# Kernel optimization log

Measured on AMD Instinct MI355X. Metric: run time of the kernel, lower is better.

## Reference

```python
import jax, jax.numpy as jnp
import numpy as np

# dims
A, T, K, H, NH, F, L = 64, 50, 6, 128, 8, 60, 512
M = A * T * K          # 19200 mode nodes (layout: agent, time, mode)
AT = A * T             # 3200 agent-timestep nodes
NL = 10                # GA layers: t2m,l2m,m2m_h,m2m_a,m2m_s,t2n,l2n,n2n_h,n2n_a,n2n_s
FF = 4 * H
E = 150000


def _ln(x, g, b):
    mu = x.mean(-1, keepdims=True)
    var = jnp.mean((x - mu) ** 2, axis=-1, keepdims=True)
    return (x - mu) * jax.lax.rsqrt(var + 1e-5) * g + b


def _mlp(x, W1, b1, W2, b2):
    return jax.nn.relu(x @ W1 + b1) @ W2 + b2


def _edge_emb(attr, i, eW1, eb1, eW2, eb2):
    # pad raw edge features to width 5 so all embed MLPs share a stacked param layout
    x = jnp.pad(attr, ((0, 0), (0, 5 - attr.shape[-1])))
    return jax.nn.relu(x @ eW1[i] + eb1[i]) @ eW2[i] + eb2[i]


def _segment_softmax(scores, dst, n):
    smax = jax.ops.segment_max(scores, dst, num_segments=n)
    smax = jnp.where(jnp.isfinite(smax), smax, 0.0)
    ex = jnp.exp(scores - smax[dst])
    den = jax.ops.segment_sum(ex, dst, num_segments=n)
    return ex / (den[dst] + 1e-9)


def _graph_attention(i, x_src, x_dst, ei, edge_emb, p):
    (Wq, Wk, Wv, Wo, Wke, Wve, g1, b1, g2, b2, fW1, fb1, fW2, fb2) = p
    src, dst = ei[0], ei[1]
    dh = H // NH
    n_dst = x_dst.shape[0]
    xd = _ln(x_dst, g1[i], b1[i])
    xs = _ln(x_src, g1[i], b1[i])
    q = (xd @ Wq[i]).reshape(n_dst, NH, dh)
    k = (xs @ Wk[i])[src]            # gather per-edge keys  [E,H]
    v = (xs @ Wv[i])[src]
    if edge_emb is not None:
        k = k + edge_emb @ Wke[i]
        v = v + edge_emb @ Wve[i]
    k = k.reshape(-1, NH, dh)
    v = v.reshape(-1, NH, dh)
    scores = jnp.sum(q[dst] * k, axis=-1) / np.sqrt(dh)   # [E,NH]
    attn = _segment_softmax(scores, dst, n_dst)
    agg = jax.ops.segment_sum(attn[..., None] * v, dst, num_segments=n_dst)
    x = x_dst + agg.reshape(n_dst, H) @ Wo[i]
    h = _ln(x, g2[i], b2[i])
    return x + _mlp(h, fW1[i], fb1[i], fW2[i], fb2[i])


def _forward(a_input, l_embs, mode_tokens,
             emb_W1, emb_b1, emb_W2, emb_b2,
             ga_Wq, ga_Wk, ga_Wv, ga_Wo, ga_Wke, ga_Wve,
             ga_g1, ga_b1, ga_g2, ga_b2, ga_fW1, ga_fb1, ga_fW2, ga_fb2,
             tp_W1, tp_b1, tp_W2, tp_b2,
             pa_W1, pa_b1, pa_W2, pa_b2,
             tr_W1, tr_b1, tr_W2, tr_b2,
             t2m_attr, l2m_attr, m2m_h_attr, m2m_a_attr,
             t2m_ei, l2m_ei, m2m_h_ei, m2m_a_ei, m2m_s_ei):
    ga = (ga_Wq, ga_Wk, ga_Wv, ga_Wo, ga_Wke, ga_Wve,
          ga_g1, ga_b1, ga_g2, ga_b2, ga_fW1, ga_fb1, ga_fW2, ga_fb2)
    # agent embedding: TwoLayerMLP on [vel_len, vel_theta, length, width, type]
    a_embs = (jax.nn.relu(a_input @ emb_W1[0] + emb_b1[0]) @ emb_W2[0] + emb_b2[0]).reshape(AT, H)
    # mode tokens broadcast over (agent, time)
    m = jnp.broadcast_to(mode_tokens, (A, T, K, H)).reshape(M, H)
    # edge-attr embeddings (gather-compute pattern)
    t2m_e = _edge_emb(t2m_attr, 1, emb_W1, emb_b1, emb_W2, emb_b2)
    l2m_e = _edge_emb(l2m_attr, 2, emb_W1, emb_b1, emb_W2, emb_b2)
    m2m_h_e = _edge_emb(m2m_h_attr, 3, emb_W1, emb_b1, emb_W2, emb_b2)
    m2m_a_e = _edge_emb(m2m_a_attr, 4, emb_W1, emb_b1, emb_W2, emb_b2)
    # proposal stage
    m = _graph_attention(0, a_embs, m, t2m_ei, t2m_e, ga)
    m = _graph_attention(1, l_embs, m, l2m_ei, l2m_e, ga)
    m = _graph_attention(2, m, m, m2m_h_ei, m2m_h_e, ga)
    m = _graph_attention(3, m, m, m2m_a_ei, m2m_a_e, ga)
    m = _graph_attention(4, m, m, m2m_s_ei, None, ga)
    m_last = m.reshape(A, T, K, H)[:, -1]                 # [A,K,H]
    proposal = _mlp(m_last, tp_W1, tp_b1, tp_W2, tp_b2)   # [A,K,2F]
    anchor = _mlp(proposal, pa_W1, pa_b1, pa_W2, pa_b2)   # [A,K,H]
    # refinement stage on anchor-conditioned mode nodes
    n = (m.reshape(A, T, K, H) + anchor[:, None]).reshape(M, H)
    n = _graph_attention(5, a_embs, n, t2m_ei, t2m_e, ga)
    n = _graph_attention(6, l_embs, n, l2m_ei, l2m_e, ga)
    n = _graph_attention(7, n, n, m2m_h_ei, m2m_h_e, ga)
    n = _graph_attention(8, n, n, m2m_a_ei, m2m_a_e, ga)
    n = _graph_attention(9, n, n, m2m_s_ei, None, ga)
    n_last = n.reshape(A, T, K, H)[:, -1]
    refine = proposal + _mlp(n_last, tr_W1, tr_b1, tr_W2, tr_b2)
    return jnp.stack([proposal, refine])                  # [2,A,K,2F]


def setup_inputs() -> dict:
    key = jax.random.key(0)
    ks = list(jax.random.split(key, 64))
    it = iter(ks)
    nx = lambda: next(it)
    p = lambda *s: 0.02 * jax.random.normal(nx(), s, dtype=jnp.float32)
    inp = {}
    inp['a_input'] = jax.random.normal(nx(), (A, T, 5), dtype=jnp.float32)
    inp['l_embs'] = jax.random.normal(nx(), (L, H), dtype=jnp.float32)
    inp['mode_tokens'] = p(K, H)
    # stacked edge/feature embed MLPs: 0:a,1:t2m,2:l2m,3:m2m_h,4:m2m_a
    inp['emb_W1'] = p(5, 5, H); inp['emb_b1'] = jnp.zeros((5, H), jnp.float32)
    inp['emb_W2'] = p(5, H, H); inp['emb_b2'] = jnp.zeros((5, H), jnp.float32)
    # stacked GraphAttention params
    for nm in ['ga_Wq', 'ga_Wk', 'ga_Wv', 'ga_Wo', 'ga_Wke', 'ga_Wve']:
        inp[nm] = p(NL, H, H)
    inp['ga_g1'] = jnp.ones((NL, H), jnp.float32); inp['ga_b1'] = jnp.zeros((NL, H), jnp.float32)
    inp['ga_g2'] = jnp.ones((NL, H), jnp.float32); inp['ga_b2'] = jnp.zeros((NL, H), jnp.float32)
    inp['ga_fW1'] = p(NL, H, FF); inp['ga_fb1'] = jnp.zeros((NL, FF), jnp.float32)
    inp['ga_fW2'] = p(NL, FF, H); inp['ga_fb2'] = jnp.zeros((NL, H), jnp.float32)
    # heads
    inp['tp_W1'] = p(H, H); inp['tp_b1'] = jnp.zeros((H,), jnp.float32)
    inp['tp_W2'] = p(H, 2 * F); inp['tp_b2'] = jnp.zeros((2 * F,), jnp.float32)
    inp['pa_W1'] = p(2 * F, H); inp['pa_b1'] = jnp.zeros((H,), jnp.float32)
    inp['pa_W2'] = p(H, H); inp['pa_b2'] = jnp.zeros((H,), jnp.float32)
    inp['tr_W1'] = p(H, H); inp['tr_b1'] = jnp.zeros((H,), jnp.float32)
    inp['tr_W2'] = p(H, 2 * F); inp['tr_b2'] = jnp.zeros((2 * F,), jnp.float32)
    # raw edge features
    inp['t2m_attr'] = jax.random.normal(nx(), (E, 4), dtype=jnp.float32)
    inp['l2m_attr'] = jax.random.normal(nx(), (E, 3), dtype=jnp.float32)
    inp['m2m_h_attr'] = jax.random.normal(nx(), (E, 4), dtype=jnp.float32)
    inp['m2m_a_attr'] = jax.random.normal(nx(), (E, 3), dtype=jnp.float32)
    # edge indices (src row range differs per graph)
    ri = lambda hi: jax.random.randint(nx(), (E,), 0, hi, dtype=jnp.int32)
    inp['t2m_ei'] = jnp.stack([ri(AT), ri(M)])
    inp['l2m_ei'] = jnp.stack([ri(L), ri(M)])
    inp['m2m_h_ei'] = jnp.stack([ri(M), ri(M)])
    inp['m2m_a_ei'] = jnp.stack([ri(M), ri(M)])
    inp['m2m_s_ei'] = jnp.stack([ri(M), ri(M)])
    return inp


def reference(a_input, l_embs, mode_tokens,
              emb_W1, emb_b1, emb_W2, emb_b2,
              ga_Wq, ga_Wk, ga_Wv, ga_Wo, ga_Wke, ga_Wve,
              ga_g1, ga_b1, ga_g2, ga_b2, ga_fW1, ga_fb1, ga_fW2, ga_fb2,
              tp_W1, tp_b1, tp_W2, tp_b2,
              pa_W1, pa_b1, pa_W2, pa_b2,
              tr_W1, tr_b1, tr_W2, tr_b2,
              t2m_attr, l2m_attr, m2m_h_attr, m2m_a_attr,
              t2m_ei, l2m_ei, m2m_h_ei, m2m_a_ei, m2m_s_ei):
    return _forward(a_input, l_embs, mode_tokens,
                    emb_W1, emb_b1, emb_W2, emb_b2,
                    ga_Wq, ga_Wk, ga_Wv, ga_Wo, ga_Wke, ga_Wve,
                    ga_g1, ga_b1, ga_g2, ga_b2, ga_fW1, ga_fb1, ga_fW2, ga_fb2,
                    tp_W1, tp_b1, tp_W2, tp_b2,
                    pa_W1, pa_b1, pa_W2, pa_b2,
                    tr_W1, tr_b1, tr_W2, tr_b2,
                    t2m_attr, l2m_attr, m2m_h_attr, m2m_a_attr,
                    t2m_ei, l2m_ei, m2m_h_ei, m2m_a_ei, m2m_s_ei)
```

## Files before the change

kernel.cpp:

```cpp
#include <hip/hip_runtime.h>
#include <hip/hip_bf16.h>
#include <math.h>

#define DEV __device__ __forceinline__

typedef __attribute__((ext_vector_type(4))) float floatx4;
typedef __attribute__((ext_vector_type(8))) __bf16 bf16x8;

static constexpr int A_ = 64, T_ = 50, K_ = 6, H_ = 128, NH_ = 8, F_ = 60, L_ = 512;
static constexpr int M_  = A_ * T_ * K_;
static constexpr int AT_ = A_ * T_;
static constexpr int FF_ = 4 * H_;
static constexpr int NL_ = 10;
static constexpr int P2F = 2 * F_;
static constexpr int AK_ = A_ * K_;
static constexpr size_t WLAY = 196608;

DEV ushort f2bh(float f) {
    unsigned u = __float_as_uint(f);
    unsigned r = u + 0x7FFFu + ((u >> 16) & 1u);
    return (ushort)(r >> 16);
}
DEV float bh2f(ushort h) { return __uint_as_float(((unsigned)h) << 16); }

__global__ __launch_bounds__(256) void ln_kernel(const float* __restrict__ x,
                                                 const float* __restrict__ g,
                                                 const float* __restrict__ b,
                                                 float* __restrict__ y, int n) {
    int row = blockIdx.x * 4 + (threadIdx.x >> 6);
    int lane = threadIdx.x & 63;
    if (row >= n) return;
    const float* xr = x + (size_t)row * H_;
    float v0 = xr[lane], v1 = xr[lane + 64];
    float s = v0 + v1;
    for (int m = 32; m >= 1; m >>= 1) s += __shfl_xor(s, m, 64);
    float mu = s * (1.f / 128.f);
    float d0 = v0 - mu, d1 = v1 - mu;
    float vs = d0 * d0 + d1 * d1;
    for (int m = 32; m >= 1; m >>= 1) vs += __shfl_xor(vs, m, 64);
    float rs = rsqrtf(vs * (1.f / 128.f) + 1e-5f);
    float* yr = y + (size_t)row * H_;
    yr[lane]      = d0 * rs * g[lane] + b[lane];
    yr[lane + 64] = d1 * rs * g[lane + 64] + b[lane + 64];
}

template <int ACT, bool RES>
__global__ __launch_bounds__(256) void mgemm(const float* __restrict__ X,
                                             const ushort* __restrict__ Wh,
                                             const ushort* __restrict__ Wl,
                                             const float* __restrict__ bias,
                                             const float* __restrict__ res,
                                             float* __restrict__ Y,
                                             int n, int Kd, int C) {
    __shared__ ushort lds[4 * 8192];
    ushort* Xh  = lds;
    ushort* Xl  = lds + 8192;
    ushort* Wsh = lds + 16384;
    ushort* Wsl = lds + 24576;
    int row0 = blockIdx.x * 128, col0 = blockIdx.y * 128;
    int tid = threadIdx.x;
    int lane = tid & 63, wid = tid >> 6;
    int rbase = (wid >> 1) * 64, cbase = (wid & 1) * 64;
    int lrow = lane & 15, lk = lane >> 4;
    floatx4 acc[4][4];
#pragma unroll
    for (int a = 0; a < 4; a++)
#pragma unroll
        for (int b2 = 0; b2 < 4; b2++) acc[a][b2] = floatx4{0.f, 0.f, 0.f, 0.f};

    for (int k0 = 0; k0 < Kd; k0 += 64) {
#pragma unroll
        for (int i = 0; i < 8; i++) {
            int idx = tid + i * 256;
            int r = idx >> 4, kc = idx & 15;
            float4 v = *(const float4*)(X + (size_t)(row0 + r) * Kd + k0 + kc * 4);
            ushort h0 = f2bh(v.x), h1 = f2bh(v.y), h2 = f2bh(v.z), h3 = f2bh(v.w);
            ushort l0 = f2bh(v.x - bh2f(h0)), l1 = f2bh(v.y - bh2f(h1)),
                   l2 = f2bh(v.z - bh2f(h2)), l3 = f2bh(v.w - bh2f(h3));
            int base = (r << 6) + (((kc >> 1) ^ (r & 7)) << 3) + ((kc & 1) << 2);
            *(ushort4*)(Xh + base) = make_ushort4(h0, h1, h2, h3);
            *(ushort4*)(Xl + base) = make_ushort4(l0, l1, l2, l3);
        }
#pragma unroll
        for (int i = 0; i < 4; i++) {
            int idx = tid + i * 256;
            int c = idx >> 3, ch = idx & 7;
            int base = (c << 6) + ((ch ^ (c & 7)) << 3);
            size_t go = (size_t)(col0 + c) * Kd + k0 + ch * 8;
            *(float4*)(Wsh + base) = *(const float4*)(Wh + go);
            *(float4*)(Wsl + base) = *(const float4*)(Wl + go);
        }
        __syncthreads();
#pragma unroll
        for (int kk = 0; kk < 2; kk++) {
            int ch = kk * 4 + lk;
            bf16x8 xh[4], xl[4], wh[4], wl[4];
#pragma unroll
            for (int s = 0; s < 4; s++) {
                int r = rbase + s * 16 + lrow;
                int xoff = (r << 6) + ((ch ^ (r & 7)) << 3);
                xh[s] = *(const bf16x8*)(Xh + xoff);
                xl[s] = *(const bf16x8*)(Xl + xoff);
                int c = cbase + s * 16 + lrow;
                int woff = (c << 6) + ((ch ^ (c & 7)) << 3);
                wh[s] = *(const bf16x8*)(Wsh + woff);
                wl[s] = *(const bf16x8*)(Wsl + woff);
            }
#pragma unroll
            for (int sr = 0; sr < 4; sr++)
#pragma unroll
                for (int sc = 0; sc < 4; sc++) {
                    acc[sr][sc] = __builtin_amdgcn_mfma_f32_16x16x32_bf16(wh[sc], xh[sr], acc[sr][sc], 0, 0, 0);
                    acc[sr][sc] = __builtin_amdgcn_mfma_f32_16x16x32_bf16(wl[sc], xh[sr], acc[sr][sc], 0, 0, 0);
                    acc[sr][sc] = __builtin_amdgcn_mfma_f32_16x16x32_bf16(wh[sc], xl[sr], acc[sr][sc], 0, 0, 0);
                }
        }
        __syncthreads();
    }
#pragma unroll
    for (int sr = 0; sr < 4; sr++) {
        int row = row0 + rbase + sr * 16 + lrow;
#pragma unroll
        for (int sc = 0; sc < 4; sc++) {
            int col = col0 + cbase + sc * 16 + lk * 4;
            size_t o = (size_t)row * C + col;
            float4 v = make_float4(acc[sr][sc][0], acc[sr][sc][1],
                                   acc[sr][sc][2], acc[sr][sc][3]);
            if (bias) { float4 bv = *(const float4*)(bias + col);
                        v.x += bv.x; v.y += bv.y; v.z += bv.z; v.w += bv.w; }
            if (ACT == 1) { v.x = fmaxf(v.x, 0.f); v.y = fmaxf(v.y, 0.f);
                            v.z = fmaxf(v.z, 0.f); v.w = fmaxf(v.w, 0.f); }
            if (RES) { float4 rv = *(const float4*)(res + o);
                       v.x += rv.x; v.y += rv.y; v.z += rv.z; v.w += rv.w; }
            *(float4*)(Y + o) = v;
        }
    }
}

__global__ __launch_bounds__(256) void prep_w(const float* __restrict__ Wq,
                                              const float* __restrict__ Wk,
                                              const float* __restrict__ Wv,
                                              const float* __restrict__ Wo,
                                              const float* __restrict__ fW1,
                                              const float* __restrict__ fW2,
                                              ushort* __restrict__ oh,
                                              ushort* __restrict__ ol) {
    int l = blockIdx.y, t = blockIdx.x;
    const float* src; int K, C, tiles_c; size_t obase;
    if (t < 64) {
        int mi = t >> 4; t &= 15;
        src = (mi == 0 ? Wq : mi == 1 ? Wk : mi == 2 ? Wv : Wo) + (size_t)l * 16384;
        K = 128; C = 128; tiles_c = 4; obase = (size_t)l * WLAY + (size_t)mi * 16384;
    } else if (t < 128) {
        t -= 64; src = fW1 + (size_t)l * 65536;
        K = 128; C = 512; tiles_c = 16; obase = (size_t)l * WLAY + 65536;
    } else {
        t -= 128; src = fW2 + (size_t)l * 65536;
        K = 512; C = 128; tiles_c = 4; obase = (size_t)l * WLAY + 131072;
    }
    int tc = t % tiles_c, tk = t / tiles_c;
    __shared__ float tile[32][33];
    int tx = threadIdx.x & 31, ty = threadIdx.x >> 5;
#pragma unroll
    for (int i = 0; i < 4; i++) {
        int k = tk * 32 + ty + i * 8;
        tile[ty + i * 8][tx] = src[(size_t)k * C + tc * 32 + tx];
    }
    __syncthreads();
#pragma unroll
    for (int i = 0; i < 4; i++) {
        int c = tc * 32 + ty + i * 8;
        float v = tile[tx][ty + i * 8];
        ushort h = f2bh(v);
        ushort lo = f2bh(v - bh2f(h));
        size_t o = obase + (size_t)c * K + tk * 32 + tx;
        oh[o] = h; ol[o] = lo;
    }
}

template <int ACT, bool RES>
__global__ void small_gemm(const float* __restrict__ X, const float* __restrict__ W,
                           const float* __restrict__ bias, const float* __restrict__ res,
                           float* __restrict__ Y, int n, int Kd, int C) {
    int idx = blockIdx.x * 256 + threadIdx.x;
    if (idx >= n * C) return;
    int row = idx / C, c = idx - row * C;
    float a = bias ? bias[c] : 0.f;
    const float* xr = X + (size_t)row * Kd;
    for (int k = 0; k < Kd; k++) a = fmaf(xr[k], W[(size_t)k * C + c], a);
    if (ACT == 1) a = fmaxf(a, 0.f);
    if (RES) a += res[idx];
    Y[idx] = a;
}

__global__ __launch_bounds__(256) void combine_fast(const float* __restrict__ eW2,
                                                    const float* __restrict__ Wke,
                                                    const float* __restrict__ Wve,
                                                    float* __restrict__ cW) {
    __shared__ float Xs[128 * 36];
    __shared__ float Ws[32 * 128];
    int x = blockIdx.x;
    int li = x & 7, kv = x >> 3;
    int l = li < 4 ? li : li + 1;
    int g = (li & 3) + 1;
    const float* E2 = eW2 + (size_t)g * 16384;
    const float* Wp = (kv ? Wve : Wke) + (size_t)l * 16384;
    float* out = cW + (size_t)l * 32768 + kv * 128;
    int tid = threadIdx.x;
    int tc = tid & 15, tr = tid >> 4;
    int cA = tc * 4, rA = tr * 4;
    float acc[8][8] = {};
    for (int j0 = 0; j0 < 128; j0 += 32) {
#pragma unroll
        for (int i = 0; i < 4; i++) {
            int idx = tid + i * 256;
            int r = idx >> 3, jc = idx & 7;
            *(float4*)(Xs + r * 36 + jc * 4) =
                *(const float4*)(E2 + (size_t)r * 128 + j0 + jc * 4);
        }
#pragma unroll
        for (int i = 0; i < 4; i++) {
            int idx = tid + i * 256;
            int cc = idx & 31, jj = idx >> 5;
            *(float4*)(Ws + jj * 128 + cc * 4) =
                *(const float4*)(Wp + (size_t)(j0 + jj) * 128 + cc * 4);
        }
        __syncthreads();
#pragma unroll 8
        for (int jj = 0; jj < 32; jj++) {
            float4 w0 = *(const float4*)(Ws + jj * 128 + cA);
            float4 w1 = *(const float4*)(Ws + jj * 128 + cA + 64);
            float xr[8];
#pragma unroll
            for (int i2 = 0; i2 < 4; i2++) {
                xr[i2]     = Xs[(rA + i2) * 36 + jj];
                xr[4 + i2] = Xs[(rA + i2 + 64) * 36 + jj];
            }
#pragma unroll
            for (int i2 = 0; i2 < 8; i2++) {
                float xv = xr[i2];
                acc[i2][0] = fmaf(xv, w0.x, acc[i2][0]);
                acc[i2][1] = fmaf(xv, w0.y, acc[i2][1]);
                acc[i2][2] = fmaf(xv, w0.z, acc[i2][2]);
                acc[i2][3] = fmaf(xv, w0.w, acc[i2][3]);
                acc[i2][4] = fmaf(xv, w1.x, acc[i2][4]);
                acc[i2][5] = fmaf(xv, w1.y, acc[i2][5]);
                acc[i2][6] = fmaf(xv, w1.z, acc[i2][6]);
                acc[i2][7] = fmaf(xv, w1.w, acc[i2][7]);
            }
        }
        __syncthreads();
    }
#pragma unroll
    for (int i = 0; i < 8; i++) {
        int r = (i < 4) ? (rA + i) : (rA + i + 60);
#pragma unroll
        for (int chh = 0; chh < 2; chh++) {
            int c = cA + chh * 64;
            *(float4*)(out + (size_t)r * 256 + c) =
                make_float4(acc[i][chh * 4 + 0], acc[i][chh * 4 + 1],
                            acc[i][chh * 4 + 2], acc[i][chh * 4 + 3]);
        }
    }
}
__global__ void combine_bias(const float* __restrict__ eb2,
                             const float* __restrict__ Wke,
                             const float* __restrict__ Wve,
                             float* __restrict__ cb) {
    int x = blockIdx.x;
    int li = x & 7, kv = x >> 3;
    int l = li < 4 ? li : li + 1;
    int g = (li & 3) + 1;
    const float* Wp = (kv ? Wve : Wke) + (size_t)l * 16384;
    const float* eb = eb2 + g * 128;
    int cc = threadIdx.x;
    float a = 0.f;
    for (int j = 0; j < 128; j++) a = fmaf(eb[j], Wp[(size_t)j * 128 + cc], a);
    cb[l * 256 + kv * 128 + cc] = a;
}

__global__ void zero_i32(int* __restrict__ p, int n) {
    int i = blockIdx.x * 256 + threadIdx.x;
    if (i < n) p[i] = 0;
}
__global__ void hist_kernel(const int* __restrict__ dst, int E, int* __restrict__ deg) {
    int e = blockIdx.x * 256 + threadIdx.x;
    if (e < E) atomicAdd(&deg[dst[e]], 1);
}
__global__ __launch_bounds__(256) void exscan5(const int* __restrict__ deg0,
                                               int* __restrict__ off0,
                                               int* __restrict__ cursor0, int n) {
    int g = blockIdx.x;
    const int* deg = deg0 + (size_t)g * n;
    int* off = off0 + (size_t)g * (n + 1);
    int* cursor = cursor0 + (size_t)g * n;
    __shared__ int wsum[4];
    __shared__ int carry;
    int tid = threadIdx.x, lane = tid & 63, w = tid >> 6;
    if (tid == 0) carry = 0;
    __syncthreads();
    for (int base = 0; base < n; base += 256) {
        int v = (base + tid < n) ? deg[base + tid] : 0;
        int incl = v;
        for (int d = 1; d < 64; d <<= 1) {
            int t = __shfl_up(incl, d, 64);
            if (lane >= d) incl += t;
        }
        if (lane == 63) wsum[w] = incl;
        __syncthreads();
        int woff = 0;
        for (int i = 0; i < w; i++) woff += wsum[i];
        int total = wsum[0] + wsum[1] + wsum[2] + wsum[3];
        int excl = carry + woff + incl - v;
        if (base + tid < n) { off[base + tid] = excl; cursor[base + tid] = excl; }
        __syncthreads();
        if (tid == 0) carry += total;
        __syncthreads();
    }
    if (threadIdx.x == 0) off[n] = carry;
}
__global__ void scatter_kernel(const int* __restrict__ dst, int E,
                               int* __restrict__ cursor, int* __restrict__ eids) {
    int e = blockIdx.x * 256 + threadIdx.x;
    if (e < E) { int p = atomicAdd(&cursor[dst[e]], 1); eids[p] = e; }
}
__global__ void sort_edges(const int* __restrict__ eid, const int* __restrict__ srcArr,
                           const float* __restrict__ attr, int aw, int E,
                           int* __restrict__ esrc, float4* __restrict__ eattr) {
    int pos = blockIdx.x * 256 + threadIdx.x;
    if (pos >= E) return;
    int e = eid[pos];
    esrc[pos] = srcArr[e];
    if (attr) {
        float4 v;
        v.x = attr[(size_t)e * aw + 0];
        v.y = attr[(size_t)e * aw + 1];
        v.z = (aw > 2) ? attr[(size_t)e * aw + 2] : 0.f;
        v.w = (aw > 3) ? attr[(size_t)e * aw + 3] : 0.f;
        eattr[pos] = v;
    }
}

__global__ __launch_bounds__(256) void prep_g(const float* __restrict__ q,
                                              const float* __restrict__ cWl,
                                              const float* __restrict__ cbl,
                                              ushort* __restrict__ g,
                                              float* __restrict__ sb) {
    __shared__ float Cks[128 * 132];
    __shared__ float qs[128];
    int tid = threadIdx.x;
    {
        int cp = tid >> 1, cb0 = (tid & 1) * 64;
#pragma unroll
        for (int kq = 0; kq < 16; kq++)
            *(float4*)(Cks + cp * 132 + cb0 + kq * 4) =
                *(const float4*)(cWl + (size_t)cp * 256 + cb0 + kq * 4);
    }
    int cp = tid & 127, hb = (tid >> 7) * 4;
    for (int d = blockIdx.x; d < M_; d += gridDim.x) {
        __syncthreads();
        if (tid < 32) *(float4*)(qs + tid * 4) = *(const float4*)(q + (size_t)d * 128 + tid * 4);
        __syncthreads();
#pragma unroll
        for (int h = hb; h < hb + 4; h++) {
            float a = 0.f;
#pragma unroll
            for (int jq = 0; jq < 4; jq++) {
                float4 ck = *(float4*)(Cks + cp * 132 + h * 16 + jq * 4);
                float4 qv = *(float4*)(qs + h * 16 + jq * 4);
                a = fmaf(ck.x, qv.x, a); a = fmaf(ck.y, qv.y, a);
                a = fmaf(ck.z, qv.z, a); a = fmaf(ck.w, qv.w, a);
            }
            g[(size_t)d * 1024 + h * 128 + cp] = f2bh(a * 0.25f);
        }
        if (tid < 8) {
            float a = 0.f;
#pragma unroll
            for (int t16 = 0; t16 < 16; t16++)
                a = fmaf(cbl[tid * 16 + t16], qs[tid * 16 + t16], a);
            sb[d * 8 + tid] = a * 0.25f;
        }
    }
}

__global__ __launch_bounds__(256) void attn_fact(const int* __restrict__ off,
                                                 const int* __restrict__ esrc,
                                                 const float4* __restrict__ eattr,
                                                 const ushort* __restrict__ g,
                                                 const float* __restrict__ sb,
                                                 const float* __restrict__ eW1,
                                                 const float* __restrict__ eb1,
                                                 const float* __restrict__ kx,
                                                 const float* __restrict__ vx,
                                                 const float* __restrict__ q,
                                                 ushort* __restrict__ hsum,
                                                 float* __restrict__ vxacc,
                                                 float* __restrict__ den) {
    __shared__ float lds[4 * 144];
    int w = threadIdx.x >> 6, l = threadIdx.x & 63;
    int i = l & 15, hlo = l >> 4;
    float* hw = lds + w * 144;
    int d = blockIdx.x * 4 + w;
    int beg = off[d], end = off[d + 1];
    float q0 = q[(size_t)d * 128 + l] * 0.25f;
    float q1 = q[(size_t)d * 128 + 64 + l] * 0.25f;
    float gA[8], gB[8];
#pragma unroll
    for (int j = 0; j < 8; j++) {
        gA[j] = bh2f(g[(size_t)d * 1024 + hlo * 128 + j * 16 + i]);
        gB[j] = bh2f(g[(size_t)d * 1024 + (hlo + 4) * 128 + j * 16 + i]);
    }
    float sbA = sb[d * 8 + hlo], sbB = sb[d * 8 + 4 + hlo];
    float w1a[4], w1b[4];
#pragma unroll
    for (int j = 0; j < 4; j++) { w1a[j] = eW1[j * 128 + l]; w1b[j] = eW1[j * 128 + 64 + l]; }
    float ebA = eb1[l], ebB = eb1[64 + l];
    float mA = -INFINITY, mB = -INFINITY, dnA = 0.f, dnB = 0.f;
    float accL[8] = {}, accH[8] = {};
    float va0 = 0.f, va1 = 0.f;
    float4 aC = make_float4(0.f, 0.f, 0.f, 0.f);
    float k0C = 0.f, k1C = 0.f, v0C = 0.f, v1C = 0.f;
    if (beg < end) {
        int s0 = esrc[beg]; aC = eattr[beg];
        const float* kxr = kx + (size_t)s0 * 128;
        const float* vxr = vx + (size_t)s0 * 128;
        k0C = kxr[l]; k1C = kxr[64 + l];
        v0C = vxr[l]; v1C = vxr[64 + l];
    }
    for (int pos = beg; pos < end; pos++) {
        float4 at = aC;
        float k0 = k0C, k1 = k1C, v0 = v0C, v1 = v1C;
        if (pos + 1 < end) {
            int sN = esrc[pos + 1]; aC = eattr[pos + 1];
            const float* kxr = kx + (size_t)sN * 128;
            const float* vxr = vx + (size_t)sN * 128;
            k0C = kxr[l]; k1C = kxr[64 + l];
            v0C = vxr[l]; v1C = vxr[64 + l];
        }
        float h0 = fmaxf(ebA + at.x * w1a[0] + at.y * w1a[1] + at.z * w1a[2] + at.w * w1a[3], 0.f);
        float h1 = fmaxf(ebB + at.x * w1b[0] + at.y * w1b[1] + at.z * w1b[2] + at.w * w1b[3], 0.f);
        hw[l] = h0; hw[64 + l] = h1;
        __builtin_amdgcn_wave_barrier();
        float pA = q0 * k0, pB = q1 * k1;
#pragma unroll
        for (int j = 0; j < 8; j++) {
            float hv = hw[j * 16 + i];
            pA = fmaf(hv, gA[j], pA);
            pB = fmaf(hv, gB[j], pB);
        }
#pragma unroll
        for (int msk = 1; msk < 16; msk <<= 1) {
            pA += __shfl_xor(pA, msk, 64);
            pB += __shfl_xor(pB, msk, 64);
        }
        pA += sbA; pB += sbB;
        float nmA = fmaxf(mA, pA), nmB = fmaxf(mB, pB);
        float cA = __expf(mA - nmA), cB = __expf(mB - nmB);
        float wA = __expf(pA - nmA), wB = __expf(pB - nmB);
        mA = nmA; mB = nmB;
        dnA = dnA * cA + wA; dnB = dnB * cB + wB;
        va0 = va0 * cA + wA * v0; va1 = va1 * cB + wB * v1;
        if (i == 0) {
            hw[128 + hlo] = wA; hw[132 + hlo] = wB;
            hw[136 + hlo] = cA; hw[140 + hlo] = cB;
        }
        __builtin_amdgcn_wave_barrier();
        float4 wv0 = *(float4*)(hw + 128), wv1 = *(float4*)(hw + 132);
        float4 cv0 = *(float4*)(hw + 136), cv1 = *(float4*)(hw + 140);
        accL[0] = fmaf(accL[0], cv0.x, wv0.x * h0); accH[0] = fmaf(accH[0], cv0.x, wv0.x * h1);
        accL[1] = fmaf(accL[1], cv0.y, wv0.y * h0); accH[1] = fmaf(accH[1], cv0.y, wv0.y * h1);
        accL[2] = fmaf(accL[2], cv0.z, wv0.z * h0); accH[2] = fmaf(accH[2], cv0.z, wv0.z * h1);
        accL[3] = fmaf(accL[3], cv0.w, wv0.w * h0); accH[3] = fmaf(accH[3], cv0.w, wv0.w * h1);
        accL[4] = fmaf(accL[4], cv1.x, wv1.x * h0); accH[4] = fmaf(accH[4], cv1.x, wv1.x * h1);
        accL[5] = fmaf(accL[5], cv1.y, wv1.y * h0); accH[5] = fmaf(accH[5], cv1.y, wv1.y * h1);
        accL[6] = fmaf(accL[6], cv1.z, wv1.z * h0); accH[6] = fmaf(accH[6], cv1.z, wv1.z * h1);
        accL[7] = fmaf(accL[7], cv1.w, wv1.w * h0); accH[7] = fmaf(accH[7], cv1.w, wv1.w * h1);
    }
#pragma unroll
    for (int h = 0; h < 8; h++) {
        hsum[(size_t)d * 1024 + h * 128 + l]      = f2bh(accL[h]);
        hsum[(size_t)d * 1024 + h * 128 + 64 + l] = f2bh(accH[h]);
    }
    vxacc[(size_t)d * 128 + l] = va0;
    vxacc[(size_t)d * 128 + 64 + l] = va1;
    if (i == 0) { den[d * 8 + hlo] = dnA; den[d * 8 + 4 + hlo] = dnB; }
}

__global__ __launch_bounds__(256) void attn_plain(const int* __restrict__ off,
                                                  const int* __restrict__ esrc,
                                                  const float* __restrict__ kx,
                                                  const float* __restrict__ vx,
                                                  const float* __restrict__ q,
                                                  float* __restrict__ agg) {
    int w = threadIdx.x >> 6, lane = threadIdx.x & 63;
    int d = blockIdx.x * 4 + w;
    int beg = off[d], end = off[d + 1];
    float q0 = q[(size_t)d * 128 + lane] * 0.25f;
    float q1 = q[(size_t)d * 128 + 64 + lane] * 0.25f;
    float m0 = -INFINITY, m1 = -INFINITY;
    float den0 = 0.f, den1 = 0.f, acc0 = 0.f, acc1 = 0.f;
    float k0C = 0.f, k1C = 0.f, v0C = 0.f, v1C = 0.f;
    if (beg < end) {
        int s0 = esrc[beg];
        const float* kxr = kx + (size_t)s0 * 128;
        const float* vxr = vx + (size_t)s0 * 128;
        k0C = kxr[lane]; k1C = kxr[64 + lane];
        v0C = vxr[lane]; v1C = vxr[64 + lane];
    }
    for (int pos = beg; pos < end; pos++) {
        float k0 = k0C, k1 = k1C, v0 = v0C, v1 = v1C;
        if (pos + 1 < end) {
            int sN = esrc[pos + 1];
            const float* kxr = kx + (size_t)sN * 128;
            const float* vxr = vx + (size_t)sN * 128;
            k0C = kxr[lane]; k1C = kxr[64 + lane];
            v0C = vxr[lane]; v1C = vxr[64 + lane];
        }
        float p0 = q0 * k0, p1 = q1 * k1;
#pragma unroll
        for (int msk = 1; msk < 16; msk <<= 1) {
            p0 += __shfl_xor(p0, msk, 64);
            p1 += __shfl_xor(p1, msk, 64);
        }
        float nm0 = fmaxf(m0, p0), nm1 = fmaxf(m1, p1);
        float c0 = __expf(m0 - nm0), c1 = __expf(m1 - nm1);
        float e0 = __expf(p0 - nm0), e1 = __expf(p1 - nm1);
        acc0 = acc0 * c0 + e0 * v0; den0 = den0 * c0 + e0;
        acc1 = acc1 * c1 + e1 * v1; den1 = den1 * c1 + e1;
        m0 = nm0; m1 = nm1;
    }
    agg[(size_t)d * 128 + lane]      = acc0 / (den0 + 1e-9f);
    agg[(size_t)d * 128 + 64 + lane] = acc1 / (den1 + 1e-9f);
}

static constexpr int HST_ = 1092;
__global__ __launch_bounds__(256) void agg_fin(const ushort* __restrict__ hsum,
                                               const float* __restrict__ vxacc,
                                               const float* __restrict__ den,
                                               const float* __restrict__ cWl,
                                               const float* __restrict__ cbl,
                                               float* __restrict__ agg) {
    __shared__ float Cvs[128 * 128];
    __shared__ float hstage[8 * HST_];
    __shared__ float dens[64];
    int tid = threadIdx.x;
    {
        int cp = tid >> 1, cb0 = (tid & 1) * 64;
#pragma unroll
        for (int kq = 0; kq < 16; kq++)
            *(float4*)(Cvs + cp * 128 + cb0 + kq * 4) =
                *(const float4*)(cWl + (size_t)cp * 256 + 128 + cb0 + kq * 4);
    }
    int j = tid & 31, dsel = tid >> 5;
    int c4 = j * 4, h = j >> 2;
    float4 cvb = *(const float4*)(cbl + 128 + c4);
    for (int d0 = blockIdx.x * 8; d0 < M_; d0 += gridDim.x * 8) {
        __syncthreads();
        int r = tid * 4;
#pragma unroll
        for (int k = 0; k < 8; k++) {
            ushort4 u = *(const ushort4*)(hsum + (size_t)(d0 + k) * 1024 + r);
            *(float4*)(hstage + k * HST_ + (r >> 7) * 136 + (r & 127)) =
                make_float4(bh2f(u.x), bh2f(u.y), bh2f(u.z), bh2f(u.w));
        }
        if (tid < 64) dens[tid] = den[d0 * 8 + tid];
        __syncthreads();
        int d = d0 + dsel;
        float dn = dens[dsel * 8 + h];
        float inv = 1.f / (dn + 1e-9f);
        float cf = dn * inv;
        float a0 = 0.f, a1 = 0.f, a2 = 0.f, a3 = 0.f;
        const float* hrow = hstage + dsel * HST_ + h * 136;
#pragma unroll 4
        for (int cpp = 0; cpp < 128; cpp++) {
            float hs = hrow[cpp];
            float4 cv = *(float4*)(Cvs + cpp * 128 + c4);
            a0 = fmaf(hs, cv.x, a0); a1 = fmaf(hs, cv.y, a1);
            a2 = fmaf(hs, cv.z, a2); a3 = fmaf(hs, cv.w, a3);
        }
        float4 vv = *(const float4*)(vxacc + (size_t)d * 128 + c4);
        float4 o;
        o.x = (vv.x + a0) * inv + cvb.x * cf;
        o.y = (vv.y + a1) * inv + cvb.y * cf;
        o.z = (vv.z + a2) * inv + cvb.z * cf;
        o.w = (vv.w + a3) * inv + cvb.w * cf;
        *(float4*)(agg + (size_t)d * 128 + c4) = o;
    }
}

__global__ void mode_init(float* __restrict__ m, const float* __restrict__ mt) {
    int idx = blockIdx.x * 256 + threadIdx.x;
    if (idx >= M_ * H_) return;
    int node = idx >> 7, c = idx & 127;
    m[idx] = mt[(node % K_) * H_ + c];
}
__global__ void extract_last(const float* __restrict__ m, float* __restrict__ out) {
    int idx = blockIdx.x * 256 + threadIdx.x;
    if (idx >= AK_ * H_) return;
    int row = idx >> 7, c = idx & 127;
    int a = row / K_, k = row - a * K_;
    int node = (a * T_ + (T_ - 1)) * K_ + k;
    out[idx] = m[(size_t)node * H_ + c];
}
__global__ void add_anchor(float* __restrict__ m, const float* __restrict__ anchor) {
    int idx = blockIdx.x * 256 + threadIdx.x;
    if (idx >= M_ * H_) return;
    int node = idx >> 7, c = idx & 127;
    int a = node / (T_ * K_), k = node % K_;
    m[idx] += anchor[(size_t)(a * K_ + k) * H_ + c];
}

extern "C" void kernel_launch(void* const* d_in, const int* in_sizes, int n_in,
                              void* d_out, int out_size, void* d_ws, size_t ws_size,
                              hipStream_t stream) {
    const float* a_input     = (const float*)d_in[0];
    const float* l_embs      = (const float*)d_in[1];
    const float* mode_tokens = (const float*)d_in[2];
    const float* emb_W1 = (const float*)d_in[3];
    const float* emb_b1 = (const float*)d_in[4];
    const float* emb_W2 = (const float*)d_in[5];
    const float* emb_b2 = (const float*)d_in[6];
    const float* ga_Wq  = (const float*)d_in[7];
    const float* ga_Wk  = (const float*)d_in[8];
    const float* ga_Wv  = (const float*)d_in[9];
    const float* ga_Wo  = (const float*)d_in[10];
    const float* ga_Wke = (const float*)d_in[11];
    const float* ga_Wve = (const float*)d_in[12];
    const float* ga_g1  = (const float*)d_in[13];
    const float* ga_b1  = (const float*)d_in[14];
    const float* ga_g2  = (const float*)d_in[15];
    const float* ga_b2  = (const float*)d_in[16];
    const float* ga_fW1 = (const float*)d_in[17];
    const float* ga_fb1 = (const float*)d_in[18];
    const float* ga_fW2 = (const float*)d_in[19];
    const float* ga_fb2 = (const float*)d_in[20];
    const float* tp_W1 = (const float*)d_in[21];
    const float* tp_b1 = (const float*)d_in[22];
    const float* tp_W2 = (const float*)d_in[23];
    const float* tp_b2 = (const float*)d_in[24];
    const float* pa_W1 = (const float*)d_in[25];
    const float* pa_b1 = (const float*)d_in[26];
    const float* pa_W2 = (const float*)d_in[27];
    const float* pa_b2 = (const float*)d_in[28];
    const float* tr_W1 = (const float*)d_in[29];
    const float* tr_b1 = (const float*)d_in[30];
    const float* tr_W2 = (const float*)d_in[31];
    const float* tr_b2 = (const float*)d_in[32];
    const float* attrs[4] = { (const float*)d_in[33], (const float*)d_in[34],
                              (const float*)d_in[35], (const float*)d_in[36] };
    const int* eis[5] = { (const int*)d_in[37], (const int*)d_in[38], (const int*)d_in[39],
                          (const int*)d_in[40], (const int*)d_in[41] };
    int Es[5];
    int Emax = 0;
    for (int i = 0; i < 5; i++) { Es[i] = in_sizes[37 + i] / 2; if (Es[i] > Emax) Emax = Es[i]; }

    size_t off = 0;
    auto alloc = [&](size_t nbytes) -> char* {
        char* p = (char*)d_ws + off;
        off += ((nbytes + 255) / 256) * 256;
        return p;
    };
    float* cW     = (float*)alloc((size_t)NL_ * 128 * 256 * 4);
    float* cb     = (float*)alloc((size_t)NL_ * 256 * 4);
    ushort* wbh   = (ushort*)alloc((size_t)NL_ * WLAY * 2);
    ushort* wbl   = (ushort*)alloc((size_t)NL_ * WLAY * 2);
    float* a_embs = (float*)alloc((size_t)AT_ * H_ * 4);
    float* m      = (float*)alloc((size_t)M_ * H_ * 4);
    float* xd_ln  = (float*)alloc((size_t)M_ * H_ * 4);
    float* xs_ln  = (float*)alloc((size_t)AT_ * H_ * 4);
    float* q      = (float*)alloc((size_t)M_ * H_ * 4);
    float* kx     = (float*)alloc((size_t)M_ * H_ * 4);
    float* vx     = (float*)alloc((size_t)M_ * H_ * 4);
    float* agg    = (float*)alloc((size_t)M_ * H_ * 4);
    float* big    = (float*)alloc((size_t)M_ * FF_ * 4);
    ushort* gbuf  = (ushort*)alloc((size_t)M_ * 1024 * 2);
    ushort* hsumb = (ushort*)alloc((size_t)M_ * 1024 * 2);
    float* vxacc  = (float*)alloc((size_t)M_ * H_ * 4);
    float* den    = (float*)alloc((size_t)M_ * 8 * 4);
    float* sb     = (float*)alloc((size_t)M_ * 8 * 4);
    int* csr_off  = (int*)alloc((size_t)5 * (M_ + 1) * 4);
    int* csr_eid  = (int*)alloc((size_t)5 * Emax * 4);
    int* esrc     = (int*)alloc((size_t)5 * Emax * 4);
    float4* eattr = (float4*)alloc((size_t)4 * Emax * 16);
    int* deg5     = (int*)alloc((size_t)5 * M_ * 4);
    int* cursor5  = (int*)alloc((size_t)5 * M_ * 4);
    float* mlast  = (float*)alloc((size_t)AK_ * H_ * 4);
    float* hbuf   = (float*)alloc((size_t)AK_ * H_ * 4);
    float* anchor = (float*)alloc((size_t)AK_ * H_ * 4);
    (void)ws_size; (void)n_in;

    float* outp = (float*)d_out;

    zero_i32<<<(5 * M_ + 255) / 256, 256, 0, stream>>>(deg5, 5 * M_);
    for (int gI = 0; gI < 5; gI++)
        hist_kernel<<<(Es[gI] + 255) / 256, 256, 0, stream>>>(eis[gI] + Es[gI], Es[gI], deg5 + (size_t)gI * M_);
    exscan5<<<5, 256, 0, stream>>>(deg5, csr_off, cursor5, M_);
    for (int gI = 0; gI < 5; gI++)
        scatter_kernel<<<(Es[gI] + 255) / 256, 256, 0, stream>>>(eis[gI] + Es[gI], Es[gI],
            cursor5 + (size_t)gI * M_, csr_eid + (size_t)gI * Emax);
    for (int gI = 0; gI < 5; gI++) {
        int aw = (gI == 0 || gI == 2) ? 4 : (gI == 4 ? 0 : 3);
        sort_edges<<<(Es[gI] + 255) / 256, 256, 0, stream>>>(
            csr_eid + (size_t)gI * Emax, eis[gI], (gI < 4) ? attrs[gI] : nullptr, aw, Es[gI],
            esrc + (size_t)gI * Emax, eattr + (size_t)gI * Emax);
    }

    prep_w<<<dim3(192, 10), 256, 0, stream>>>(ga_Wq, ga_Wk, ga_Wv, ga_Wo, ga_fW1, ga_fW2, wbh, wbl);
    combine_fast<<<16, 256, 0, stream>>>(emb_W2, ga_Wke, ga_Wve, cW);
    combine_bias<<<16, 128, 0, stream>>>(emb_b2, ga_Wke, ga_Wve, cb);

    small_gemm<1, false><<<(AT_ * H_ + 255) / 256, 256, 0, stream>>>(a_input, emb_W1, emb_b1, nullptr, big, AT_, 5, H_);
    small_gemm<0, false><<<(AT_ * H_ + 255) / 256, 256, 0, stream>>>(big, emb_W2, emb_b2, nullptr, a_embs, AT_, H_, H_);
    mode_init<<<(M_ * H_ + 255) / 256, 256, 0, stream>>>(m, mode_tokens);

    struct Cfg { const float* srcX; int n_src; int gi; bool hasE; };
    Cfg cfgs[10] = {
        { a_embs, AT_, 0, true }, { l_embs, L_, 1, true },
        { nullptr, M_, 2, true }, { nullptr, M_, 3, true },
        { nullptr, M_, 4, false },
        { a_embs, AT_, 0, true }, { l_embs, L_, 1, true },
        { nullptr, M_, 2, true }, { nullptr, M_, 3, true },
        { nullptr, M_, 4, false },
    };

    for (int l = 0; l < 10; l++) {
        const Cfg& cf = cfgs[l];
        const int* offg = csr_off + cf.gi * (M_ + 1);
        const int* esrcg = esrc + (size_t)cf.gi * Emax;
        const float4* eattrg = eattr + (size_t)cf.gi * Emax;
        const float* g1 = ga_g1 + l * H_; const float* b1 = ga_b1 + l * H_;
        size_t wb = (size_t)l * WLAY;

        ln_kernel<<<M_ / 4, 256, 0, stream>>>(m, g1, b1, xd_ln, M_);
        mgemm<0, false><<<dim3(M_ / 128, 1), 256, 0, stream>>>(
            xd_ln, wbh + wb, wbl + wb, nullptr, nullptr, q, M_, 128, 128);
        const float* srcLN = xd_ln;
        if (cf.srcX) {
            ln_kernel<<<cf.n_src / 4, 256, 0, stream>>>(cf.srcX, g1, b1, xs_ln, cf.n_src);
            srcLN = xs_ln;
        }
        mgemm<0, false><<<dim3(cf.n_src / 128, 1), 256, 0, stream>>>(
            srcLN, wbh + wb + 16384, wbl + wb + 16384, nullptr, nullptr, kx, cf.n_src, 128, 128);
        mgemm<0, false><<<dim3(cf.n_src / 128, 1), 256, 0, stream>>>(
            srcLN, wbh + wb + 32768, wbl + wb + 32768, nullptr, nullptr, vx, cf.n_src, 128, 128);

        if (cf.hasE) {
            int gg = (l < 5) ? l + 1 : l - 4;
            const float* eW1g = emb_W1 + (size_t)gg * 5 * H_;
            const float* eb1g = emb_b1 + (size_t)gg * H_;
            prep_g<<<2400, 256, 0, stream>>>(q, cW + (size_t)l * 128 * 256, cb + l * 256, gbuf, sb);
            attn_fact<<<M_ / 4, 256, 0, stream>>>(offg, esrcg, eattrg, gbuf, sb, eW1g, eb1g,
                                                  kx, vx, q, hsumb, vxacc, den);
            agg_fin<<<256, 256, 0, stream>>>(hsumb, vxacc, den,
                                             cW + (size_t)l * 128 * 256, cb + l * 256, agg);
        } else {
            attn_plain<<<M_ / 4, 256, 0, stream>>>(offg, esrcg, kx, vx, q, agg);
        }

        mgemm<0, true><<<dim3(M_ / 128, 1), 256, 0, stream>>>(
            agg, wbh + wb + 49152, wbl + wb + 49152, nullptr, m, m, M_, 128, 128);
        ln_kernel<<<M_ / 4, 256, 0, stream>>>(m, ga_g2 + l * H_, ga_b2 + l * H_, xd_ln, M_);
        mgemm<1, false><<<dim3(M_ / 128, 4), 256, 0, stream>>>(
            xd_ln, wbh + wb + 65536, wbl + wb + 65536, ga_fb1 + l * FF_, nullptr, big, M_, 128, 512);
        mgemm<0, true><<<dim3(M_ / 128, 1), 256, 0, stream>>>(
            big, wbh + wb + 131072, wbl + wb + 131072, ga_fb2 + l * H_, m, m, M_, 512, 128);

        if (l == 4) {
            extract_last<<<(AK_ * H_ + 255) / 256, 256, 0, stream>>>(m, mlast);
            small_gemm<1, false><<<(AK_ * H_ + 255) / 256, 256, 0, stream>>>(mlast, tp_W1, tp_b1, nullptr, hbuf, AK_, H_, H_);
            small_gemm<0, false><<<(AK_ * P2F + 255) / 256, 256, 0, stream>>>(hbuf, tp_W2, tp_b2, nullptr, outp, AK_, H_, P2F);
            small_gemm<1, false><<<(AK_ * H_ + 255) / 256, 256, 0, stream>>>(outp, pa_W1, pa_b1, nullptr, hbuf, AK_, P2F, H_);
            small_gemm<0, false><<<(AK_ * H_ + 255) / 256, 256, 0, stream>>>(hbuf, pa_W2, pa_b2, nullptr, anchor, AK_, H_, H_);
            add_anchor<<<(M_ * H_ + 255) / 256, 256, 0, stream>>>(m, anchor);
        }
    }

    extract_last<<<(AK_ * H_ + 255) / 256, 256, 0, stream>>>(m, mlast);
    small_gemm<1, false><<<(AK_ * H_ + 255) / 256, 256, 0, stream>>>(mlast, tr_W1, tr_b1, nullptr, hbuf, AK_, H_, H_);
    small_gemm<0, true><<<(AK_ * P2F + 255) / 256, 256, 0, stream>>>(hbuf, tr_W2, tr_b2, outp, outp + AK_ * P2F, AK_, H_, P2F);
}
```

Baseline: 2.829 ms.

## Keep prep_g weights in registers, batch 8 rows per block, transpose g layout

prep_g no longer stages the full 128x128 weight slice into a 66KB shared buffer and loops over rows with two barriers per row. Each thread now holds its 64 weight values in registers, and each block handles 8 destination rows with a single barrier. The g buffer layout is transposed to [cp][h] so each thread writes its four head outputs as one ushort4, and attn_fact's read indexing is updated to match. The cost is higher register pressure from the 64-float array, plus attn_fact loads that may now be strided.

```diff
diff --git a/kernel.cpp b/kernel.cpp
--- a/kernel.cpp
+++ b/kernel.cpp
@@ -346,40 +346,48 @@
                                               const float* __restrict__ cbl,
                                               ushort* __restrict__ g,
                                               float* __restrict__ sb) {
-    __shared__ float Cks[128 * 132];
-    __shared__ float qs[128];
+    __shared__ float qs[8 * 132];
     int tid = threadIdx.x;
+    int cp = tid & 127, hb = (tid >> 7) * 4;
+    float ck[64];
     {
-        int cp = tid >> 1, cb0 = (tid & 1) * 64;
-#pragma unroll
-        for (int kq = 0; kq < 16; kq++)
-            *(float4*)(Cks + cp * 132 + cb0 + kq * 4) =
-                *(const float4*)(cWl + (size_t)cp * 256 + cb0 + kq * 4);
-    }
-    int cp = tid & 127, hb = (tid >> 7) * 4;
-    for (int d = blockIdx.x; d < M_; d += gridDim.x) {
-        __syncthreads();
-        if (tid < 32) *(float4*)(qs + tid * 4) = *(const float4*)(q + (size_t)d * 128 + tid * 4);
-        __syncthreads();
-#pragma unroll
-        for (int h = hb; h < hb + 4; h++) {
-            float a = 0.f;
-#pragma unroll
-            for (int jq = 0; jq < 4; jq++) {
-                float4 ck = *(float4*)(Cks + cp * 132 + h * 16 + jq * 4);
-                float4 qv = *(float4*)(qs + h * 16 + jq * 4);
-                a = fmaf(ck.x, qv.x, a); a = fmaf(ck.y, qv.y, a);
-                a = fmaf(ck.z, qv.z, a); a = fmaf(ck.w, qv.w, a);
-            }
-            g[(size_t)d * 1024 + h * 128 + cp] = f2bh(a * 0.25f);
-        }
-        if (tid < 8) {
-            float a = 0.f;
-#pragma unroll
-            for (int t16 = 0; t16 < 16; t16++)
-                a = fmaf(cbl[tid * 16 + t16], qs[tid * 16 + t16], a);
-            sb[d * 8 + tid] = a * 0.25f;
-        }
+        const float* csrc = cWl + (size_t)cp * 256 + hb * 16;
+#pragma unroll
+        for (int t4 = 0; t4 < 16; t4++) {
+            float4 v = *(const float4*)(csrc + t4 * 4);
+            ck[t4 * 4 + 0] = v.x; ck[t4 * 4 + 1] = v.y;
+            ck[t4 * 4 + 2] = v.z; ck[t4 * 4 + 3] = v.w;
+        }
+    }
+    int d0 = blockIdx.x * 8;
+    {
+        int dl = tid >> 5, col = (tid & 31) * 4;
+        *(float4*)(qs + dl * 132 + col) = *(const float4*)(q + (size_t)(d0 + dl) * 128 + col);
+    }
+    __syncthreads();
+#pragma unroll
+    for (int dl = 0; dl < 8; dl++) {
+        const float* qr = qs + dl * 132 + hb * 16;
+        float a0 = 0.f, a1 = 0.f, a2 = 0.f, a3 = 0.f;
+#pragma unroll
+        for (int t = 0; t < 16; t++) {
+            a0 = fmaf(ck[t],      qr[t],      a0);
+            a1 = fmaf(ck[16 + t], qr[16 + t], a1);
+            a2 = fmaf(ck[32 + t], qr[32 + t], a2);
+            a3 = fmaf(ck[48 + t], qr[48 + t], a3);
+        }
+        ushort4 o = make_ushort4(f2bh(a0 * 0.25f), f2bh(a1 * 0.25f),
+                                 f2bh(a2 * 0.25f), f2bh(a3 * 0.25f));
+        *(ushort4*)(g + (size_t)(d0 + dl) * 1024 + cp * 8 + hb) = o;
+    }
+    if (tid < 64) {
+        int dl = tid >> 3, h = tid & 7;
+        const float* qr = qs + dl * 132 + h * 16;
+        const float* cbr = cbl + h * 16;
+        float a = 0.f;
+#pragma unroll
+        for (int t = 0; t < 16; t++) a = fmaf(cbr[t], qr[t], a);
+        sb[(d0 + dl) * 8 + h] = a * 0.25f;
     }
 }
 
@@ -407,8 +415,8 @@
     float gA[8], gB[8];
 #pragma unroll
     for (int j = 0; j < 8; j++) {
-        gA[j] = bh2f(g[(size_t)d * 1024 + hlo * 128 + j * 16 + i]);
-        gB[j] = bh2f(g[(size_t)d * 1024 + (hlo + 4) * 128 + j * 16 + i]);
+        gA[j] = bh2f(g[(size_t)d * 1024 + (j * 16 + i) * 8 + hlo]);
+        gB[j] = bh2f(g[(size_t)d * 1024 + (j * 16 + i) * 8 + hlo + 4]);
     }
     float sbA = sb[d * 8 + hlo], sbB = sb[d * 8 + 4 + hlo];
     float w1a[4], w1b[4];
@@ -748,7 +756,7 @@
             int gg = (l < 5) ? l + 1 : l - 4;
             const float* eW1g = emb_W1 + (size_t)gg * 5 * H_;
             const float* eb1g = emb_b1 + (size_t)gg * H_;
-            prep_g<<<2400, 256, 0, stream>>>(q, cW + (size_t)l * 128 * 256, cb + l * 256, gbuf, sb);
+            prep_g<<<M_ / 8, 256, 0, stream>>>(q, cW + (size_t)l * 128 * 256, cb + l * 256, gbuf, sb);
             attn_fact<<<M_ / 4, 256, 0, stream>>>(offg, esrcg, eattrg, gbuf, sb, eW1g, eb1g,
                                                   kx, vx, q, hsumb, vxacc, den);
             agg_fin<<<256, 256, 0, stream>>>(hsumb, vxacc, den,
```

New measurement: 2.694 ms. 4.8% less time.
